# Performance work log

Hardware: AMD Instinct MI355X
Metric: run time of the kernel (lower is better)

The kernel has to match this reference:

```python
import jax, jax.numpy as jnp
import numpy as np

NUM_HEADS = 16
NUM_KV_HEADS = 4
ROPE_BASE = 10000.0
TRAIN_SEQ_LEN = 2048


def _rms_norm(x):
    eps = jnp.asarray(jnp.finfo(x.dtype).eps, x.dtype)
    return x * jax.lax.rsqrt(jnp.mean(x * x, axis=-1, keepdims=True) + eps)


def _rope_cos_sin(seq_len, head_dim, dtype):
    # seq_len <= TRAIN_SEQ_LEN -> no NTK rescaling, matches Rotary buffer path
    half = head_dim // 2
    inv_freq = 1.0 / (ROPE_BASE ** (jnp.arange(0, head_dim, 2, dtype=jnp.float32) / head_dim))
    t = jnp.arange(seq_len, dtype=jnp.float32)
    freqs = jnp.outer(t, inv_freq)  # [S, half]
    cos = jnp.cos(freqs)[None, :, None, :].astype(dtype)
    sin = jnp.sin(freqs)[None, :, None, :].astype(dtype)
    return cos, sin


def _apply_rotary(x, cos, sin):
    half = x.shape[-1] // 2
    x1, x2 = x[..., :half], x[..., half:]
    return jnp.concatenate([x1 * cos + x2 * sin, -x1 * sin + x2 * cos], axis=-1)


def setup_inputs() -> dict:
    key = jax.random.key(0)
    ks = jax.random.split(key, 5)
    B, S, D = 2, 2048, 2048
    kv_dim = NUM_KV_HEADS * (D // NUM_HEADS)
    sw = 0.02
    return {
        "x": jax.random.normal(ks[0], (B, S, D), jnp.float32),
        "Wq": jax.random.normal(ks[1], (D, D), jnp.float32) * sw,
        "Wk": jax.random.normal(ks[2], (kv_dim, D), jnp.float32) * sw,
        "Wv": jax.random.normal(ks[3], (kv_dim, D), jnp.float32) * sw,
        "Wproj": jax.random.normal(ks[4], (D, D), jnp.float32) * sw,
        "q_gain": jnp.ones((NUM_HEADS,), jnp.float32),
    }


def reference(x, Wq, Wk, Wv, Wproj, q_gain):
    B, S, D = x.shape
    H, Hkv = NUM_HEADS, NUM_KV_HEADS
    hd = D // H
    r = H // Hkv

    q = (x @ Wq.T).reshape(B, S, H, hd)
    k = (x @ Wk.T).reshape(B, S, Hkv, hd)
    v = (x @ Wv.T).reshape(B, S, Hkv, hd)

    q = _rms_norm(q)
    k = _rms_norm(k)

    cos, sin = _rope_cos_sin(S, hd, q.dtype)
    q = _apply_rotary(q, cos, sin)
    k = _apply_rotary(k, cos, sin)
    q = q * q_gain.astype(q.dtype)[None, None, :, None]

    # GQA: repeat kv heads (repeat_interleave along head dim)
    k = jnp.repeat(k, r, axis=2)  # [B,S,H,hd]
    v = jnp.repeat(v, r, axis=2)

    scale = 1.0 / jnp.sqrt(jnp.asarray(hd, q.dtype))
    scores = jnp.einsum("bqhd,bkhd->bhqk", q, k) * scale
    causal = jnp.tril(jnp.ones((S, S), dtype=bool))
    scores = jnp.where(causal[None, None], scores, jnp.asarray(-jnp.inf, scores.dtype))
    attn = jax.nn.softmax(scores, axis=-1)
    y = jnp.einsum("bhqk,bkhd->bqhd", attn, v)

    return y.reshape(B, S, D) @ Wproj.T
```

## Files before the change

kernel.cpp:

```cpp
#include <hip/hip_runtime.h>

#define D_MODEL 2048
#define SEQ 2048
#define BATCH 2
#define NH 16
#define NKV 4
#define HD 128
#define KVD (NKV * HD)
#define QKVN (D_MODEL + 2 * KVD)
#define MROWS (BATCH * SEQ)

typedef __attribute__((ext_vector_type(8))) short short8;
typedef __attribute__((ext_vector_type(4))) float f32x4;

__device__ __forceinline__ unsigned short f2bf(float f) {
    union { float f; unsigned int u; } v; v.f = f;
    unsigned int r = (v.u + 0x7FFFu + ((v.u >> 16) & 1u)) >> 16;
    return (unsigned short)r;
}

__device__ __forceinline__ unsigned short f2bf_pos(float f) {
    union { float f; unsigned int u; } v; v.f = f;
    return (unsigned short)((v.u + 0x8000u) >> 16);
}

__device__ __forceinline__ float bf2f(unsigned short u) {
    union { float f; unsigned int i; } v; v.i = ((unsigned int)u) << 16;
    return v.f;
}

__device__ __forceinline__ void async16(const void* g, void* l) {
    __builtin_amdgcn_global_load_lds((const __attribute__((address_space(1))) void*)g,
                                     (__attribute__((address_space(3))) void*)l, 16, 0, 0);
}

__global__ __launch_bounds__(256) void cast_all(const float* __restrict__ x,
                                                const float* __restrict__ wq,
                                                const float* __restrict__ wk,
                                                const float* __restrict__ wv,
                                                const float* __restrict__ wp,
                                                unsigned short* __restrict__ xb,
                                                unsigned short* __restrict__ wqkv,
                                                unsigned short* __restrict__ wpb) {
    int i = blockIdx.x * 256 + threadIdx.x;
    const float4* s; ushort4* d; int j;
    if (i < 2097152)      { s = (const float4*)x;  d = (ushort4*)xb;             j = i; }
    else if (i < 3145728) { s = (const float4*)wq; d = (ushort4*)wqkv;           j = i - 2097152; }
    else if (i < 3407872) { s = (const float4*)wk; d = (ushort4*)wqkv + 1048576; j = i - 3145728; }
    else if (i < 3670016) { s = (const float4*)wv; d = (ushort4*)wqkv + 1310720; j = i - 3407872; }
    else                  { s = (const float4*)wp; d = (ushort4*)wpb;            j = i - 3670016; }
    float4 v = s[j];
    ushort4 o;
    o.x = f2bf(v.x); o.y = f2bf(v.y); o.z = f2bf(v.z); o.w = f2bf(v.w);
    d[j] = o;
}

__global__ __launch_bounds__(512) void gemm_qkv(const unsigned short* __restrict__ A,
                                                const unsigned short* __restrict__ W,
                                                const float* __restrict__ gain,
                                                unsigned short* __restrict__ qbuf,
                                                unsigned short* __restrict__ kbuf,
                                                unsigned short* __restrict__ vtb) {
    __shared__ unsigned short smem[65536];
    unsigned short* tile = smem;
    const int K = D_MODEL;
    const int tid  = threadIdx.x;
    const int lane = tid & 63;
    const int wave = tid >> 6;
    const int qm   = lane & 15;
    const int quad = lane >> 4;
    const int wr   = wave >> 2;
    const int wc   = wave & 3;
    const int lin = blockIdx.x + 12 * blockIdx.y;
    const int l2  = (lin & 7) * 24 + (lin >> 3);
    const int bx  = l2 % 12;
    const int m0  = (l2 / 12) * 256;
    const int n0 = bx * 256;

    f32x4 acc[2][2][4][2];
#pragma unroll
    for (int a = 0; a < 2; a++)
#pragma unroll
        for (int b = 0; b < 2; b++)
#pragma unroll
            for (int c = 0; c < 4; c++)
#pragma unroll
                for (int d = 0; d < 2; d++) acc[a][b][c][d] = (f32x4){0.f, 0.f, 0.f, 0.f};

    const unsigned short* Asrc = A + (size_t)(m0 + (tid >> 3)) * K + (((tid & 7) ^ ((tid >> 3) & 7)) * 8);
    const unsigned short* Bsrc = W + (size_t)(n0 + (tid >> 3)) * K + (((tid & 7) ^ ((tid >> 3) & 7)) * 8);
    const int dstg = tid * 8;
    const int ck0 = ((quad ^ (qm & 7)) * 8);
    const int ck1 = (((4 + quad) ^ (qm & 7)) * 8);
    const int arow = wr * 64 + qm;
    const int brow = wc * 32 + qm;

    short8 af[4][2], bf0[2][2], bf1[2][2];

#define STG_A(mh, bufv, kt1) \
    async16(Asrc + (size_t)((mh) * 128) * K + (kt1),      &smem[(bufv) * 16384 + (mh) * 8192 + dstg]); \
    async16(Asrc + (size_t)((mh) * 128 + 64) * K + (kt1), &smem[(bufv) * 16384 + (mh) * 8192 + 4096 + dstg]);
#define STG_B(nh, bufv, kt1) \
    async16(Bsrc + (size_t)((nh) * 128) * K + (kt1),      &smem[32768 + (bufv) * 16384 + (nh) * 8192 + dstg]); \
    async16(Bsrc + (size_t)((nh) * 128 + 64) * K + (kt1), &smem[32768 + (bufv) * 16384 + (nh) * 8192 + 4096 + dstg]);

#define RD_A(ab, mh) { \
    _Pragma("unroll") \
    for (int m = 0; m < 4; m++) { \
        af[m][0] = *(const short8*)&smem[(ab) + ((mh) * 128 + arow + m * 16) * 64 + ck0]; \
        af[m][1] = *(const short8*)&smem[(ab) + ((mh) * 128 + arow + m * 16) * 64 + ck1]; \
    } }
#define RD_B(bb, nh, dstf) { \
    _Pragma("unroll") \
    for (int n = 0; n < 2; n++) { \
        dstf[n][0] = *(const short8*)&smem[(bb) + ((nh) * 128 + brow + n * 16) * 64 + ck0]; \
        dstf[n][1] = *(const short8*)&smem[(bb) + ((nh) * 128 + brow + n * 16) * 64 + ck1]; \
    } }
#define MFMA16(mh, nh, bfr) { \
    __builtin_amdgcn_s_setprio(1); \
    _Pragma("unroll") \
    for (int m = 0; m < 4; m++) \
        _Pragma("unroll") \
        for (int n = 0; n < 2; n++) { \
            acc[mh][nh][m][n] = __builtin_amdgcn_mfma_f32_16x16x32_bf16(af[m][0], bfr[n][0], acc[mh][nh][m][n], 0, 0, 0); \
            acc[mh][nh][m][n] = __builtin_amdgcn_mfma_f32_16x16x32_bf16(af[m][1], bfr[n][1], acc[mh][nh][m][n], 0, 0, 0); \
        } \
    __builtin_amdgcn_s_setprio(0); }

#define BARv asm volatile("s_barrier" ::: "memory")
#define WV4  asm volatile("s_waitcnt vmcnt(4)" ::: "memory")
#define WV2  asm volatile("s_waitcnt vmcnt(2)" ::: "memory")
#define WV0  asm volatile("s_waitcnt vmcnt(0)" ::: "memory")

#define STEP(p, kt1) { \
     RD_A((p)*16384, 0) RD_B(32768 + (p)*16384, 0, bf0) STG_A(0, (p)^1, kt1) \
    BARv; MFMA16(0, 0, bf0) WV4; BARv; \
     RD_B(32768 + (p)*16384, 1, bf1) STG_B(0, (p)^1, kt1) \
    BARv; MFMA16(0, 1, bf1) WV4; BARv; \
     RD_A((p)*16384, 1) STG_B(1, (p)^1, kt1) \
    BARv; MFMA16(1, 0, bf0) BARv; \
     STG_A(1, (p)^1, kt1) \
    BARv; MFMA16(1, 1, bf1) WV4; BARv; \
}
#define STEPE(p) { \
    RD_A((p)*16384, 0) RD_B(32768 + (p)*16384, 0, bf0) BARv; MFMA16(0, 0, bf0) WV2; BARv; \
    RD_B(32768 + (p)*16384, 1, bf1)                    BARv; MFMA16(0, 1, bf1) WV0; BARv; \
    RD_A((p)*16384, 1)                                 BARv; MFMA16(1, 0, bf0) BARv; \
    MFMA16(1, 1, bf1) \
}

    STG_A(0, 0, 0) STG_B(0, 0, 0) STG_B(1, 0, 0) STG_A(1, 0, 0)
    WV4; BARv;

#pragma unroll 1
    for (int t2 = 0; t2 < 15; ++t2) {
        STEP(0, t2 * 128 + 64)
        STEP(1, t2 * 128 + 128)
    }
    STEP(0, 1984)
    STEPE(1)
#undef STG_A
#undef STG_B
#undef RD_A
#undef RD_B
#undef MFMA16
#undef STEP
#undef STEPE

    const int s_base = m0 & 2047;
    const int bb = m0 >> 11;
    const float invf = __builtin_amdgcn_exp2f(-(float)lane * 0.20761871f - 2.6514961f);

#pragma unroll
    for (int half = 0; half < 2; ++half) {
        __syncthreads();
#pragma unroll
        for (int nh = 0; nh < 2; nh++)
#pragma unroll
            for (int m = 0; m < 4; m++)
#pragma unroll
                for (int n = 0; n < 2; n++)
#pragma unroll
                    for (int r = 0; r < 4; r++) {
                        int row = wr * 64 + m * 16 + quad * 4 + r;
                        int col = nh * 128 + wc * 32 + n * 16 + qm;
                        tile[row * 264 + col] = f2bf(acc[half][nh][m][n][r]);
                    }
        __syncthreads();

        if (bx < 10) {
            const bool isq = bx < 8;
#pragma unroll
            for (int hh = 0; hh < 2; hh++) {
                const int h = (isq ? 2 * bx : (bx - 8) * 2) + hh;
                const float g = isq ? gain[h] * 0.12751744f : 1.0f;
                unsigned short* dst = isq
                    ? qbuf + ((size_t)(bb * NH + h) * SEQ + s_base + half * 128) * HD
                    : kbuf + ((size_t)(bb * NKV + h) * SEQ + s_base + half * 128) * HD;
                for (int rr = 0; rr < 16; rr++) {
                    int row = wave * 16 + rr;
                    float x1 = bf2f(tile[row * 264 + hh * 128 + lane]);
                    float x2 = bf2f(tile[row * 264 + hh * 128 + 64 + lane]);
                    float ss = x1 * x1 + x2 * x2;
                    ss += __shfl_xor(ss, 1);  ss += __shfl_xor(ss, 2);  ss += __shfl_xor(ss, 4);
                    ss += __shfl_xor(ss, 8);  ss += __shfl_xor(ss, 16); ss += __shfl_xor(ss, 32);
                    float rs = rsqrtf(ss * (1.0f / 128.0f) + 1.1920929e-07f);
                    float rev = (float)(s_base + half * 128 + row) * invf;
                    rev -= truncf(rev);
                    float sn = __builtin_amdgcn_sinf(rev);
                    float cs = __builtin_amdgcn_cosf(rev);
                    float a1 = x1 * rs, a2 = x2 * rs;
                    float o1 = (a1 * cs + a2 * sn) * g;
                    float o2 = (a2 * cs - a1 * sn) * g;
                    dst[(size_t)row * HD + lane]      = f2bf(o1);
                    dst[(size_t)row * HD + 64 + lane] = f2bf(o2);
                }
            }
        } else {
            const int sc = (tid & 31) * 4;
            const int d0 = tid >> 5;
#pragma unroll
            for (int hh = 0; hh < 2; hh++) {
                const int hk = (bx - 10) * 2 + hh;
                unsigned short* dstv = vtb + ((size_t)(bb * NKV + hk) * HD) * SEQ + s_base + half * 128;
#pragma unroll
                for (int i = 0; i < 8; i++) {
                    int d = d0 + 16 * i;
                    ushort4 ov;
                    ov.x = tile[(sc + 0) * 264 + hh * 128 + d];
                    ov.y = tile[(sc + 1) * 264 + hh * 128 + d];
                    ov.z = tile[(sc + 2) * 264 + hh * 128 + d];
                    ov.w = tile[(sc + 3) * 264 + hh * 128 + d];
                    *(ushort4*)(dstv + (size_t)d * SEQ + sc) = ov;
                }
            }
        }
    }
}

__global__ __launch_bounds__(512) void gemm_bt(const unsigned short* __restrict__ A,
                                               const unsigned short* __restrict__ W,
                                               float* __restrict__ C, int M, int N, int K) {
    __shared__ unsigned short smem[49152];
    const int tid  = threadIdx.x;
    const int lane = tid & 63;
    const int wave = tid >> 6;
    const int qm   = lane & 15;
    const int quad = lane >> 4;
    const int wr   = wave >> 2;
    const int wc   = wave & 3;
    const int lin = blockIdx.x + 16 * blockIdx.y;
    const int l2  = (lin & 7) * 32 + (lin >> 3);
    const int m0  = (l2 >> 4) * 256;
    const int n0  = (l2 & 15) * 128;

    f32x4 acc[2][4][2];
#pragma unroll
    for (int a = 0; a < 2; a++)
#pragma unroll
        for (int b = 0; b < 4; b++)
#pragma unroll
            for (int c = 0; c < 2; c++) acc[a][b][c] = (f32x4){0.f, 0.f, 0.f, 0.f};

    const unsigned short* Asrc = A + (size_t)(m0 + (tid >> 3)) * K + (((tid & 7) ^ ((tid >> 3) & 7)) * 8);
    const unsigned short* Bsrc = W + (size_t)(n0 + (tid >> 3)) * K + (((tid & 7) ^ ((tid >> 3) & 7)) * 8);
    const int dstg = tid * 8;
    const int ck0 = ((quad ^ (qm & 7)) * 8);
    const int ck1 = (((4 + quad) ^ (qm & 7)) * 8);
    const int arow = wr * 64 + qm;
    const int brow = wc * 32 + qm;

    short8 af[4][2], bfr[2][2];

#define STG_A2(mh, bufv, kt1) \
    async16(Asrc + (size_t)((mh) * 128) * K + (kt1),      &smem[(bufv) * 16384 + (mh) * 8192 + dstg]); \
    async16(Asrc + (size_t)((mh) * 128 + 64) * K + (kt1), &smem[(bufv) * 16384 + (mh) * 8192 + 4096 + dstg]);
#define STG_Bp(bufv, kt1) \
    async16(Bsrc + (kt1),                  &smem[32768 + (bufv) * 8192 + dstg]); \
    async16(Bsrc + (size_t)64 * K + (kt1), &smem[32768 + (bufv) * 8192 + 4096 + dstg]);

#define RD_A2(p, mh) { \
    _Pragma("unroll") \
    for (int m = 0; m < 4; m++) { \
        af[m][0] = *(const short8*)&smem[(p) * 16384 + ((mh) * 128 + arow + m * 16) * 64 + ck0]; \
        af[m][1] = *(const short8*)&smem[(p) * 16384 + ((mh) * 128 + arow + m * 16) * 64 + ck1]; \
    } }
#define RD_Bp(p) { \
    _Pragma("unroll") \
    for (int n = 0; n < 2; n++) { \
        bfr[n][0] = *(const short8*)&smem[32768 + (p) * 8192 + (brow + n * 16) * 64 + ck0]; \
        bfr[n][1] = *(const short8*)&smem[32768 + (p) * 8192 + (brow + n * 16) * 64 + ck1]; \
    } }
#define MFMA8(mh, kk) { \
    __builtin_amdgcn_s_setprio(1); \
    _Pragma("unroll") \
    for (int m = 0; m < 4; m++) \
        _Pragma("unroll") \
        for (int n = 0; n < 2; n++) \
            acc[mh][m][n] = __builtin_amdgcn_mfma_f32_16x16x32_bf16(af[m][kk], bfr[n][kk], acc[mh][m][n], 0, 0, 0); \
    __builtin_amdgcn_s_setprio(0); }

#define BARb asm volatile("s_barrier" ::: "memory")
#define WB4  asm volatile("s_waitcnt vmcnt(4)" ::: "memory")
#define WB2  asm volatile("s_waitcnt vmcnt(2)" ::: "memory")
#define WB0  asm volatile("s_waitcnt vmcnt(0)" ::: "memory")

#define STEPB(p, kt1) { \
     RD_A2(p, 0) RD_Bp(p) STG_A2(0, (p)^1, kt1) \
    BARb; MFMA8(0, 0) BARb; \
     STG_Bp((p)^1, kt1) \
    BARb; MFMA8(0, 1) WB4; BARb; \
     RD_A2(p, 1) STG_A2(1, (p)^1, kt1) \
    BARb; MFMA8(1, 0) BARb; \
     MFMA8(1, 1) WB2; BARb; \
}
#define STEPBE(p) { \
    RD_A2(p, 0) RD_Bp(p) MFMA8(0, 0) MFMA8(0, 1) \
    WB0; BARb; \
    RD_A2(p, 1) MFMA8(1, 0) MFMA8(1, 1) \
}

    STG_A2(0, 0, 0) STG_Bp(0, 0) STG_A2(1, 0, 0)
    WB2; BARb;

#pragma unroll 1
    for (int t2 = 0; t2 < 15; ++t2) {
        STEPB(0, t2 * 128 + 64)
        STEPB(1, t2 * 128 + 128)
    }
    STEPB(0, 1984)
    STEPBE(1)
#undef STG_A2
#undef STG_Bp
#undef RD_A2
#undef RD_Bp
#undef MFMA8
#undef STEPB
#undef STEPBE

#pragma unroll
    for (int mh = 0; mh < 2; mh++)
#pragma unroll
        for (int m = 0; m < 4; m++)
#pragma unroll
            for (int r = 0; r < 4; r++) {
                int row = m0 + mh * 128 + wr * 64 + m * 16 + quad * 4 + r;
                float* Crow = C + (size_t)row * N + n0 + wc * 32 + qm;
#pragma unroll
                for (int n = 0; n < 2; n++) Crow[n * 16] = acc[mh][m][n][r];
            }
}

__global__ __launch_bounds__(256, 4) void attn(const unsigned short* __restrict__ qb,
                                               const unsigned short* __restrict__ kb,
                                               const unsigned short* __restrict__ vt,
                                               const float* __restrict__ gain,
                                               unsigned short* __restrict__ y) {
    __shared__ unsigned short Ks[8192];
    __shared__ unsigned short Vs[8192];
    __shared__ unsigned short plds[4][1024];
    const int tid  = threadIdx.x;
    const int lane = tid & 63;
    const int wave = tid >> 6;
    const int bh   = blockIdx.x & 31;
    const int g4   = blockIdx.x >> 5;
    const int gg = g4 & 7;
    const int gs = g4 >> 3;
    const int qt64 = (gs == 0) ? gg : (gs == 1) ? (31 - gg) : (gs == 2) ? (8 + gg) : (23 - gg);
    const int h = bh & 15;
    const int b = bh >> 4;
    const int qm   = lane & 15;
    const int quad = lane >> 4;
    const int q0    = qt64 * 64;
    const int qrow0 = q0 + wave * 16;
    const float M = 17.0f * fabsf(gain[h]);

    const unsigned short* Qp = qb + (((size_t)(b * NH + h)) * SEQ + qrow0) * HD;
    const unsigned short* Kp = kb + ((size_t)(b * NKV + (h >> 2))) * SEQ * HD;
    const unsigned short* Vp = vt + ((size_t)(b * NKV + (h >> 2))) * HD * SEQ;

    short8 qf[4];
#pragma unroll
    for (int c = 0; c < 4; c++)
        qf[c] = *(const short8*)(Qp + qm * HD + c * 32 + quad * 8);

    f32x4 o[8];
#pragma unroll
    for (int t = 0; t < 8; t++) o[t] = (f32x4){0.f, 0.f, 0.f, 0.f};
    float lr[4] = {0.f, 0.f, 0.f, 0.f};

    const unsigned short* KsA = Kp + (size_t)(tid >> 4) * HD + (((tid & 15) ^ (tid >> 4)) & 15) * 8;
    const unsigned short* VsA = Vp + (size_t)(tid >> 3) * SEQ + (((tid & 7) ^ ((tid >> 3) & 7)) * 8);
    char* KsB = (char*)Ks + wave * 1024;
    char* VsB = (char*)Vs + wave * 1024;
    unsigned short* P = &plds[wave][0];

    const int kvend = q0 + 64;
    for (int kv0 = 0; kv0 < kvend; kv0 += 64) {
#pragma unroll
        for (int i = 0; i < 4; i++) {
            async16(KsA + (size_t)(16 * i) * HD,  KsB + i * 4096);
            async16(VsA + (size_t)(32 * i) * SEQ, VsB + i * 4096);
        }
        KsA += (size_t)64 * HD;
        VsA += 64;
        __syncthreads();

        f32x4 s[4];
#pragma unroll
        for (int g = 0; g < 4; g++) s[g] = (f32x4){0.f, 0.f, 0.f, 0.f};
        __builtin_amdgcn_s_setprio(1);
#pragma unroll
        for (int c = 0; c < 4; c++) {
#pragma unroll
            for (int g = 0; g < 4; g++) {
                short8 kf = *(const short8*)&Ks[(g * 16 + qm) * 128 + (((c * 4 + quad) ^ qm) * 8)];
                s[g] = __builtin_amdgcn_mfma_f32_16x16x32_bf16(qf[c], kf, s[g], 0, 0, 0);
            }
        }
        __builtin_amdgcn_s_setprio(0);
        if (kv0 + 63 > qrow0) {
#pragma unroll
            for (int g = 0; g < 4; g++)
#pragma unroll
                for (int r = 0; r < 4; r++) {
                    int qg = qrow0 + quad * 4 + r;
                    if (kv0 + g * 16 + qm > qg) s[g][r] = -3.0e38f;
                }
        }
        float p[4][4];
#pragma unroll
        for (int g = 0; g < 4; g++)
#pragma unroll
            for (int r = 0; r < 4; r++) {
                p[g][r] = __builtin_amdgcn_exp2f(s[g][r] - M);
                lr[r] += p[g][r];
            }
#pragma unroll
        for (int g = 0; g < 4; g++)
#pragma unroll
            for (int r = 0; r < 4; r++) {
                int rowp = quad * 4 + r;
                P[rowp * 64 + (((g * 2 + (qm >> 3)) ^ (rowp & 7)) * 8) + (qm & 7)] = f2bf_pos(p[g][r]);
            }
        short8 pa[2];
#pragma unroll
        for (int ka = 0; ka < 2; ka++)
            pa[ka] = *(const short8*)&P[qm * 64 + (((ka * 4 + quad) ^ (qm & 7)) * 8)];
        __builtin_amdgcn_s_setprio(1);
#pragma unroll
        for (int t = 0; t < 8; t++) {
#pragma unroll
            for (int ka = 0; ka < 2; ka++) {
                short8 vf = *(const short8*)&Vs[(t * 16 + qm) * 64 + (((ka * 4 + quad) ^ (qm & 7)) * 8)];
                o[t] = __builtin_amdgcn_mfma_f32_16x16x32_bf16(pa[ka], vf, o[t], 0, 0, 0);
            }
        }
        __builtin_amdgcn_s_setprio(0);
        __syncthreads();
    }
    float rl[4];
#pragma unroll
    for (int r = 0; r < 4; r++) {
        float l = lr[r];
        l += __shfl_xor(l, 1);
        l += __shfl_xor(l, 2);
        l += __shfl_xor(l, 4);
        l += __shfl_xor(l, 8);
        rl[r] = 1.0f / l;
    }
#pragma unroll
    for (int t = 0; t < 8; t++) {
#pragma unroll
        for (int r = 0; r < 4; r++) {
            size_t row = (size_t)(b * SEQ + qrow0 + quad * 4 + r);
            y[row * D_MODEL + h * HD + t * 16 + qm] = f2bf(o[t][r] * rl[r]);
        }
    }
}

extern "C" void kernel_launch(void* const* d_in, const int* in_sizes, int n_in,
                              void* d_out, int out_size, void* d_ws, size_t ws_size,
                              hipStream_t stream) {
    const float* x  = (const float*)d_in[0];
    const float* Wq = (const float*)d_in[1];
    const float* Wk = (const float*)d_in[2];
    const float* Wv = (const float*)d_in[3];
    const float* Wp = (const float*)d_in[4];
    const float* qg = (const float*)d_in[5];

    char* ws = (char*)d_ws;
    unsigned short* xb   = (unsigned short*)(ws + 0);
    unsigned short* wqkv = (unsigned short*)(ws + 16777216);
    unsigned short* wp   = (unsigned short*)(ws + 29360128);
    unsigned short* qbuf = (unsigned short*)(ws + 37748736);
    unsigned short* kbuf = (unsigned short*)(ws + 54525952);
    unsigned short* vtb  = (unsigned short*)(ws + 58720256);
    unsigned short* y    = xb;

    cast_all<<<18432, 256, 0, stream>>>(x, Wq, Wk, Wv, Wp, xb, wqkv, wp);
    gemm_qkv<<<dim3(12, 16), 512, 0, stream>>>(xb, wqkv, qg, qbuf, kbuf, vtb);
    attn<<<1024, 256, 0, stream>>>(qbuf, kbuf, vtb, qg, y);
    gemm_bt<<<dim3(16, 16), 512, 0, stream>>>(y, wp, (float*)d_out, MROWS, D_MODEL, D_MODEL);
}
```

Measured before the change: 275.1 us.

## Deepen QKV GEMM global-load pipeline to prefetch two k-tiles ahead

Switches the QKV projection GEMM main loop from a one-tile-ahead prefetch to a two-tile-ahead prefetch. The prologue issues loads for the first two k-tiles, and each step loads tile k+2 into the buffer being consumed, with vmcnt waits raised to keep more global loads in flight. The aim is to hide global memory latency better behind the MFMA work. The risk is a subtle hazard: stores into the same LDS buffer being read rely on barrier placement, and more VGPRs are held by in-flight loads.

```diff
diff --git a/kernel.cpp b/kernel.cpp
--- a/kernel.cpp
+++ b/kernel.cpp
@@ -128,44 +128,55 @@
     __builtin_amdgcn_s_setprio(0); }
 
 #define BARv asm volatile("s_barrier" ::: "memory")
+#define WV12 asm volatile("s_waitcnt vmcnt(12)" ::: "memory")
+#define WV10 asm volatile("s_waitcnt vmcnt(10)" ::: "memory")
+#define WV8  asm volatile("s_waitcnt vmcnt(8)" ::: "memory")
 #define WV4  asm volatile("s_waitcnt vmcnt(4)" ::: "memory")
 #define WV2  asm volatile("s_waitcnt vmcnt(2)" ::: "memory")
 #define WV0  asm volatile("s_waitcnt vmcnt(0)" ::: "memory")
 
-#define STEP(p, kt1) { \
-     RD_A((p)*16384, 0) RD_B(32768 + (p)*16384, 0, bf0) STG_A(0, (p)^1, kt1) \
-    BARv; MFMA16(0, 0, bf0) WV4; BARv; \
-     RD_B(32768 + (p)*16384, 1, bf1) STG_B(0, (p)^1, kt1) \
-    BARv; MFMA16(0, 1, bf1) WV4; BARv; \
-     RD_A((p)*16384, 1) STG_B(1, (p)^1, kt1) \
+#define STEP_D(p, kt2) { \
+     RD_A((p)*16384, 0) RD_B(32768 + (p)*16384, 0, bf0) \
+    BARv; MFMA16(0, 0, bf0) WV10; BARv; \
+     RD_B(32768 + (p)*16384, 1, bf1) STG_A(0, p, kt2) STG_B(0, p, kt2) \
+    BARv; MFMA16(0, 1, bf1) WV12; BARv; \
+     RD_A((p)*16384, 1) STG_B(1, p, kt2) \
     BARv; MFMA16(1, 0, bf0) BARv; \
-     STG_A(1, (p)^1, kt1) \
+     STG_A(1, p, kt2) \
+    BARv; MFMA16(1, 1, bf1) WV12; BARv; \
+}
+#define STEP_D30(p) { \
+    RD_A((p)*16384, 0) RD_B(32768 + (p)*16384, 0, bf0) BARv; MFMA16(0, 0, bf0) WV10; BARv; \
+    RD_B(32768 + (p)*16384, 1, bf1)                    BARv; MFMA16(0, 1, bf1) WV8;  BARv; \
+    RD_A((p)*16384, 1)                                 BARv; MFMA16(1, 0, bf0) BARv; \
     BARv; MFMA16(1, 1, bf1) WV4; BARv; \
 }
-#define STEPE(p) { \
+#define STEP_D31(p) { \
     RD_A((p)*16384, 0) RD_B(32768 + (p)*16384, 0, bf0) BARv; MFMA16(0, 0, bf0) WV2; BARv; \
     RD_B(32768 + (p)*16384, 1, bf1)                    BARv; MFMA16(0, 1, bf1) WV0; BARv; \
     RD_A((p)*16384, 1)                                 BARv; MFMA16(1, 0, bf0) BARv; \
     MFMA16(1, 1, bf1) \
 }
 
-    STG_A(0, 0, 0) STG_B(0, 0, 0) STG_B(1, 0, 0) STG_A(1, 0, 0)
-    WV4; BARv;
+    STG_A(0, 0, 0)  STG_B(0, 0, 0)  STG_B(1, 0, 0)  STG_A(1, 0, 0)
+    STG_A(0, 1, 64) STG_B(0, 1, 64) STG_B(1, 1, 64) STG_A(1, 1, 64)
+    WV12; BARv;
 
 #pragma unroll 1
     for (int t2 = 0; t2 < 15; ++t2) {
-        STEP(0, t2 * 128 + 64)
-        STEP(1, t2 * 128 + 128)
+        STEP_D(0, t2 * 128 + 128)
+        STEP_D(1, t2 * 128 + 192)
     }
-    STEP(0, 1984)
-    STEPE(1)
+    STEP_D30(0)
+    STEP_D31(1)
 #undef STG_A
 #undef STG_B
 #undef RD_A
 #undef RD_B
 #undef MFMA16
-#undef STEP
-#undef STEPE
+#undef STEP_D
+#undef STEP_D30
+#undef STEP_D31
 
     const int s_base = m0 & 2047;
     const int bb = m0 >> 11;
```

Result: no change. 274.9 us (-0.1%).
